# Kernel tuning notes

Measured on AMD Instinct MI355X. Metric: run time of the kernel, lower is better.

Reference implementation:

```python
import jax, jax.numpy as jnp
import numpy as np

B, S, D, H, FF = 4, 1024, 1024, 16, 4096
DH = D // H
EPS = 1e-5


def setup_inputs() -> dict:
    key = jax.random.key(0)
    ks = jax.random.split(key, 24)
    w = lambda i, shp: jax.random.normal(ks[i], shp, jnp.float32) * 0.02
    inp = {
        'tgt': jax.random.normal(ks[0], (B, S, D), jnp.float32),
        'memory': jax.random.normal(ks[1], (B, S, D), jnp.float32),
        'mask': jax.random.randint(ks[2], (B, S, S), 0, 2, jnp.int32),
        # self-attention projections (stored [in,out]; torch Linear weight transposed)
        'sa_wq': w(3, (D, D)), 'sa_bq': jnp.zeros((D,), jnp.float32),
        'sa_wk': w(4, (D, D)), 'sa_bk': jnp.zeros((D,), jnp.float32),
        'sa_wv': w(5, (D, D)), 'sa_bv': jnp.zeros((D,), jnp.float32),
        'sa_wo': w(6, (D, D)), 'sa_bo': jnp.zeros((D,), jnp.float32),
        # cross-attention projections
        'ca_wq': w(7, (D, D)), 'ca_bq': jnp.zeros((D,), jnp.float32),
        'ca_wk': w(8, (D, D)), 'ca_bk': jnp.zeros((D,), jnp.float32),
        'ca_wv': w(9, (D, D)), 'ca_bv': jnp.zeros((D,), jnp.float32),
        'ca_wo': w(10, (D, D)), 'ca_bo': jnp.zeros((D,), jnp.float32),
        # FFN
        'w1': w(11, (D, FF)), 'b1': jnp.zeros((FF,), jnp.float32),
        'w2': w(12, (FF, D)), 'b2': jnp.zeros((D,), jnp.float32),
        # LayerNorms
        'g1': jnp.ones((D,), jnp.float32), 'be1': jnp.zeros((D,), jnp.float32),
        'g2': jnp.ones((D,), jnp.float32), 'be2': jnp.zeros((D,), jnp.float32),
        'g3': jnp.ones((D,), jnp.float32), 'be3': jnp.zeros((D,), jnp.float32),
    }
    return inp


def _layernorm(x, g, b):
    m = jnp.mean(x, axis=-1, keepdims=True)
    v = jnp.mean((x - m) ** 2, axis=-1, keepdims=True)
    return (x - m) * jax.lax.rsqrt(v + EPS) * g + b


def _mha(x, y, mask, wq, bq, wk, bk, wv, bv, wo, bo):
    # chunk(h,-1)+cat(0) head-split == reshape to [B,S,H,DH]
    b_, sq, _ = x.shape
    sk = y.shape[1]
    q = (x @ wq + bq).reshape(b_, sq, H, DH)
    k = (y @ wk + bk).reshape(b_, sk, H, DH)
    v = (y @ wv + bv).reshape(b_, sk, H, DH)
    score = jnp.einsum('bqhd,bkhd->bhqk', q, k) / jnp.float32(np.sqrt(DH))
    score = score + (1.0 - mask[:, None].astype(score.dtype)) * (-1e9)
    attn = jax.nn.softmax(score, axis=-1)
    out = jnp.einsum('bhqk,bkhd->bqhd', attn, v).reshape(b_, sq, D)
    return out @ wo + bo


def reference(tgt, memory, mask,
              sa_wq, sa_bq, sa_wk, sa_bk, sa_wv, sa_bv, sa_wo, sa_bo,
              ca_wq, ca_bq, ca_wk, ca_bk, ca_wv, ca_bv, ca_wo, ca_bo,
              w1, b1, w2, b2, g1, be1, g2, be2, g3, be3):
    t = tgt + _mha(tgt, tgt, mask, sa_wq, sa_bq, sa_wk, sa_bk, sa_wv, sa_bv, sa_wo, sa_bo)
    t = _layernorm(t, g1, be1)
    t = t + _mha(t, memory, mask, ca_wq, ca_bq, ca_wk, ca_bk, ca_wv, ca_bv, ca_wo, ca_bo)
    t = _layernorm(t, g2, be2)
    t = t + (jax.nn.relu(t @ w1 + b1) @ w2 + b2)
    t = _layernorm(t, g3, be3)
    return t
```

## Files before the change

### kernel.cpp

```cpp
#include <hip/hip_runtime.h>
#include <math.h>

typedef float f32x4 __attribute__((ext_vector_type(4)));
typedef unsigned short ushort8 __attribute__((ext_vector_type(8)));
typedef unsigned short ushort4v __attribute__((ext_vector_type(4)));
typedef __bf16 bf16x8 __attribute__((ext_vector_type(8)));
typedef unsigned int u32;

__device__ __forceinline__ unsigned short f2bf(float x) {
  union { float f; unsigned u; } v; v.f = x;
  unsigned r = v.u + 0x7FFFu + ((v.u >> 16) & 1u);
  return (unsigned short)(r >> 16);
}
__device__ __forceinline__ float bf2f(unsigned short u) {
  union { unsigned u; float f; } c; c.u = ((unsigned)u) << 16; return c.f;
}

__device__ __forceinline__ f32x4 mfma16(ushort8 a, ushort8 b, f32x4 c) {
  return __builtin_amdgcn_mfma_f32_16x16x32_bf16(
      __builtin_bit_cast(bf16x8, a), __builtin_bit_cast(bf16x8, b), c, 0, 0, 0);
}

__device__ __forceinline__ void gload16(const void* g, void* l) {
  __builtin_amdgcn_global_load_lds((const __attribute__((address_space(1))) u32*)g,
                                   (__attribute__((address_space(3))) u32*)l, 16, 0, 0);
}

__device__ __forceinline__ int xcd_swz(int orig, int nwg) {
  int q = nwg >> 3, r = nwg & 7;
  int xcd = orig & 7, lid = orig >> 3;
  return (xcd < r ? xcd * (q + 1) : r * (q + 1) + (xcd - r) * q) + lid;
}

__global__ __launch_bounds__(256) void gemm_bf16_kernel(
    const unsigned short* __restrict__ A, const unsigned short* __restrict__ Bt,
    const float* __restrict__ bias, void* __restrict__ C,
    int M, int N, int K, int flags)
{
  __shared__ __align__(16) char As0[128 * 128];
  __shared__ __align__(16) char Bs0[128 * 128];
  __shared__ __align__(16) char As1[128 * 128];
  __shared__ __align__(16) char Bs1[128 * 128];
  const int gx = gridDim.x;
  const int wg = xcd_swz(blockIdx.x + gx * blockIdx.y, gx * gridDim.y);
  const int bn = wg % gx, bm = wg / gx;
  const int z = blockIdx.z;
  const int t = threadIdx.x;
  const int lane = t & 63, w = t >> 6, wm = w >> 1, wn = w & 1;
  const int l4 = lane & 15, lg = lane >> 4;
  const size_t K2 = (size_t)K * 2;

  f32x4 acc[4][4];
#pragma unroll
  for (int i = 0; i < 4; ++i)
#pragma unroll
    for (int j = 0; j < 4; ++j) acc[i][j] = f32x4{0.f, 0.f, 0.f, 0.f};

  const int lr = lane >> 3;
  const int ls = (lane & 7) ^ lr;
  const char* Ag = (const char*)A + (size_t)(bm * 128 + w * 32 + lr) * K2 + ls * 16;
  const char* Bg = (const char*)Bt + (size_t)(bn * 128 + w * 32 + lr) * K2 + ls * 16;
  const int wo = w * 4096;

  auto STAGE = [&](char* Al, char* Bl, int kt) {
    const size_t ko = (size_t)kt * 128;
#pragma unroll
    for (int i = 0; i < 4; ++i) {
      gload16(Ag + i * 8 * K2 + ko, Al + wo + i * 1024);
      gload16(Bg + i * 8 * K2 + ko, Bl + wo + i * 1024);
    }
  };
  auto COMPUTE = [&](const char* As, const char* Bs) {
#pragma unroll
    for (int ks = 0; ks < 2; ++ks) {
      const int kb = ks * 64 + lg * 16;
      ushort8 af[4], bfr[4];
#pragma unroll
      for (int mi = 0; mi < 4; ++mi) {
        int r = wm * 64 + mi * 16 + l4;
        af[mi] = *reinterpret_cast<const ushort8*>(As + r * 128 + (kb ^ ((r & 7) << 4)));
      }
#pragma unroll
      for (int ni = 0; ni < 4; ++ni) {
        int r = wn * 64 + ni * 16 + l4;
        bfr[ni] = *reinterpret_cast<const ushort8*>(Bs + r * 128 + (kb ^ ((r & 7) << 4)));
      }
#pragma unroll
      for (int mi = 0; mi < 4; ++mi)
#pragma unroll
        for (int ni = 0; ni < 4; ++ni)
          acc[mi][ni] = mfma16(af[mi], bfr[ni], acc[mi][ni]);
    }
  };

#define GWAIT(more) do { if (more) asm volatile("s_waitcnt vmcnt(8)" ::: "memory"); \
                         else      asm volatile("s_waitcnt vmcnt(0)" ::: "memory"); } while (0)

  const int nkt2 = (K >> 6) / gridDim.z;
  const int kbeg = z * nkt2, kend = kbeg + nkt2;
  STAGE(As0, Bs0, kbeg);
  STAGE(As1, Bs1, kbeg + 1);
  for (int kt = kbeg; kt < kend; kt += 2) {
    GWAIT(kt + 1 < kend);
    __builtin_amdgcn_s_barrier();
    __builtin_amdgcn_sched_barrier(0);
    COMPUTE(As0, Bs0);
    __builtin_amdgcn_s_barrier();
    __builtin_amdgcn_sched_barrier(0);
    if (kt + 2 < kend) STAGE(As0, Bs0, kt + 2);
    GWAIT(kt + 2 < kend);
    __builtin_amdgcn_s_barrier();
    __builtin_amdgcn_sched_barrier(0);
    COMPUTE(As1, Bs1);
    __builtin_amdgcn_s_barrier();
    __builtin_amdgcn_sched_barrier(0);
    if (kt + 3 < kend) STAGE(As1, Bs1, kt + 3);
  }
#undef GWAIT

  const int relu = flags & 1, obf = flags & 2;
#pragma unroll
  for (int mi = 0; mi < 4; ++mi)
#pragma unroll
    for (int ni = 0; ni < 4; ++ni) {
      int col = bn * 128 + wn * 64 + ni * 16 + l4;
      float bia = (z == 0) ? bias[col] : 0.f;
#pragma unroll
      for (int j = 0; j < 4; ++j) {
        int row = bm * 128 + wm * 64 + mi * 16 + lg * 4 + j;
        float vv = acc[mi][ni][j] + bia;
        if (relu) vv = fmaxf(vv, 0.f);
        size_t idx = (size_t)z * M * N + (size_t)row * N + col;
        if (obf) ((unsigned short*)C)[idx] = f2bf(vv);
        else     ((float*)C)[idx] = vv;
      }
    }
}

constexpr int kS = 1024, kD = 1024, kDH = 64;

__global__ __launch_bounds__(256) void attn_kernel(
    const unsigned short* __restrict__ Qg, const unsigned short* __restrict__ Kg,
    const unsigned short* __restrict__ Vg, int qs, int ks_,
    const unsigned short* __restrict__ mpack, unsigned short* __restrict__ Og)
{
  __shared__ __align__(16) char Ks0[8192];
  __shared__ __align__(16) char Ks1[8192];
  __shared__ __align__(16) char VT0[8192];
  __shared__ __align__(16) char VT1[8192];
  __shared__ __align__(16) char Ps[8192];
  const int wg = xcd_swz(blockIdx.x + 16 * (blockIdx.y + 16 * blockIdx.z), 1024);
  const int qt = wg & 15, h = (wg >> 4) & 15, b = wg >> 8;
  const int t = threadIdx.x, lane = t & 63, w = t >> 6;
  const int l4 = lane & 15, lg = lane >> 4;
  const int lr = lane >> 3, sg = (lane & 7) ^ lr;

  ushort8 q0, q1;
  {
    const unsigned short* src = Qg + (size_t)(b * kS + qt * 64 + w * 16 + l4) * qs + h * kDH;
    q0 = *reinterpret_cast<const ushort8*>(src + lg * 8);
    q1 = *reinterpret_cast<const ushort8*>(src + 32 + lg * 8);
  }
  const unsigned short* mtb = mpack + (size_t)(b * 16 + qt) * 4096 + t;

  auto stageK = [&](char* Kl, int kt) {
    const char* base = (const char*)(Kg + (size_t)(b * kS + kt * 64) * ks_ + h * kDH) + sg * 16;
    gload16(base + (size_t)(w * 16 + lr) * (ks_ * 2), Kl + w * 2048);
    gload16(base + (size_t)(w * 16 + 8 + lr) * (ks_ * 2), Kl + w * 2048 + 1024);
  };

  float m_r[4], l_p[4];
  f32x4 o[4];
#pragma unroll
  for (int j = 0; j < 4; ++j) { m_r[j] = -1e30f; l_p[j] = 0.f; }
#pragma unroll
  for (int di = 0; di < 4; ++di) o[di] = f32x4{0.f, 0.f, 0.f, 0.f};

  ushort8 vA0, vA1, vB0, vB1;
  unsigned short mA, mB;
  stageK(Ks0, 0);
  {
    const unsigned short* vsrc = Vg + (size_t)(b * kS + (t >> 2)) * ks_ + h * kDH + (t & 3) * 16;
    vA0 = *reinterpret_cast<const ushort8*>(vsrc);
    vA1 = *reinterpret_cast<const ushort8*>(vsrc + 8);
    mA = mtb[0];
  }

#define ATTN_TILE(KC, VC, KN, VC0, VC1, VN0, VN1, MCUR, MNXT, KTV)                       \
  {                                                                                      \
    asm volatile("s_waitcnt vmcnt(0)" ::: "memory");                                     \
    {       \
      int key2 = (t >> 2) * 2, c0 = (t & 3) * 16;                                        \
      _Pragma("unroll")                                                                  \
      for (int i = 0; i < 8; ++i) {                                                      \
        int dh = c0 + i;                                                                 \
        *(unsigned short*)(VC + dh * 128 +                                               \
            (key2 ^ ((dh & 7) << 4) ^ ((dh >> 4) << 5))) = VC0[i];                       \
      }                                                                                  \
      _Pragma("unroll")                                                                  \
      for (int i = 0; i < 8; ++i) {                                                      \
        int dh = c0 + 8 + i;                                                             \
        *(unsigned short*)(VC + dh * 128 +                                               \
            (key2 ^ ((dh & 7) << 4) ^ ((dh >> 4) << 5))) = VC1[i];                       \
      }                                                                                  \
    }                                                                                    \
    asm volatile("s_waitcnt lgkmcnt(0)" ::: "memory");                                   \
    __builtin_amdgcn_s_barrier();                                                        \
    __builtin_amdgcn_sched_barrier(0);                                                   \
    if ((KTV) + 1 < 16) {                  \
      stageK(KN, (KTV) + 1);                                                             \
      const unsigned short* vsrc = Vg +                                                  \
          (size_t)(b * kS + ((KTV) + 1) * 64 + (t >> 2)) * ks_ + h * kDH + (t & 3) * 16; \
      VN0 = *reinterpret_cast<const ushort8*>(vsrc);                                     \
      VN1 = *reinterpret_cast<const ushort8*>(vsrc + 8);                                 \
      MNXT = mtb[((KTV) + 1) * 256];                                                     \
    }                                                                                    \
    f32x4 sc[4];                                                                         \
    _Pragma("unroll")                                                                    \
    for (int ni = 0; ni < 4; ++ni) sc[ni] = f32x4{0.f, 0.f, 0.f, 0.f};                   \
    __builtin_amdgcn_s_setprio(1);                                                       \
    _Pragma("unroll")                                                                    \
    for (int ks = 0; ks < 2; ++ks) {                                                     \
      const int kb = ks * 64 + lg * 16;                                                  \
      ushort8 a = ks ? q1 : q0;                                                          \
      _Pragma("unroll")                                                                  \
      for (int ni = 0; ni < 4; ++ni) {                                                   \
        int kr = ni * 16 + l4;                                                           \
        ushort8 bb = *(const ushort8*)(KC + kr * 128 + (kb ^ ((kr & 7) << 4)));          \
        sc[ni] = mfma16(a, bb, sc[ni]);                                                  \
      }                                                                                  \
    }                                                                                    \
    __builtin_amdgcn_s_setprio(0);                                                       \
    const unsigned mbits_ = (unsigned)(MCUR);                                            \
    float tmax[4];                                                                       \
    _Pragma("unroll")                                                                    \
    for (int j = 0; j < 4; ++j) {                                                        \
      _Pragma("unroll")                                                                  \
      for (int ni = 0; ni < 4; ++ni)                                                     \
        if (!((mbits_ >> (ni * 4 + j)) & 1u)) sc[ni][j] = -1e9f;                         \
      tmax[j] = fmaxf(fmaxf(sc[0][j], sc[1][j]), fmaxf(sc[2][j], sc[3][j]));             \
    }                                                                                    \
    bool need = (tmax[0] > m_r[0] + 8.f) || (tmax[1] > m_r[1] + 8.f) ||                  \
                (tmax[2] > m_r[2] + 8.f) || (tmax[3] > m_r[3] + 8.f);                    \
    if (__any(need)) {                 \
      _Pragma("unroll")                                                                  \
      for (int j = 0; j < 4; ++j) {                                                      \
        tmax[j] = fmaxf(tmax[j], __shfl_xor(tmax[j], 1, 64));                            \
        tmax[j] = fmaxf(tmax[j], __shfl_xor(tmax[j], 2, 64));                            \
        tmax[j] = fmaxf(tmax[j], __shfl_xor(tmax[j], 4, 64));                            \
        tmax[j] = fmaxf(tmax[j], __shfl_xor(tmax[j], 8, 64));                            \
        float mn = fmaxf(m_r[j], tmax[j]);                                               \
        float al = exp2f(m_r[j] - mn);                                                   \
        m_r[j] = mn; l_p[j] *= al;                                                       \
        o[0][j] *= al; o[1][j] *= al; o[2][j] *= al; o[3][j] *= al;                      \
      }                                                                                  \
    }                                                                                    \
    _Pragma("unroll")                                                                    \
    for (int ni = 0; ni < 4; ++ni)                                                       \
      _Pragma("unroll")                                                                  \
      for (int j = 0; j < 4; ++j) {                                                      \
        float p = exp2f(sc[ni][j] - m_r[j]);                                             \
        sc[ni][j] = p;                                                                   \
        l_p[j] += p;                                                                     \
      }                                                                                  \
    {                               \
      char* Pw = Ps + w * 2048;                                                          \
      _Pragma("unroll")                                                                  \
      for (int ni = 0; ni < 4; ++ni)                                                     \
        _Pragma("unroll")                                                                \
        for (int j = 0; j < 4; ++j) {                                                    \
          int row = lg * 4 + j, col = ni * 16 + l4;                                      \
          *(unsigned short*)(Pw + row * 128 +                                            \
              ((col * 2) ^ ((row & 7) << 4) ^ ((row & 8) << 2))) =                       \
              __builtin_bit_cast(unsigned short, (__bf16)sc[ni][j]);                     \
        }                                                                                \
    }                                                                                    \
    asm volatile("s_waitcnt lgkmcnt(0)" ::: "memory");                                   \
    __builtin_amdgcn_sched_barrier(0);                                                   \
    __builtin_amdgcn_s_setprio(1);                                                       \
    {                      \
      const char* Pw = Ps + w * 2048;                                                    \
      _Pragma("unroll")                                                                  \
      for (int ks = 0; ks < 2; ++ks) {                                                   \
        const int kb = ks * 64 + lg * 16;                                                \
        ushort8 pa = *(const ushort8*)(Pw + l4 * 128 +                                   \
            (kb ^ ((l4 & 7) << 4) ^ ((l4 & 8) << 2)));                                   \
        _Pragma("unroll")                                                                \
        for (int di = 0; di < 4; ++di) {                                                 \
          int vr2 = di * 16 + l4;                                                        \
          ushort8 vb = *(const ushort8*)(VC + vr2 * 128 +                                \
              (kb ^ ((vr2 & 7) << 4) ^ ((vr2 >> 4) << 5)));                              \
          o[di] = mfma16(pa, vb, o[di]);                                                 \
        }                                                                                \
      }                                                                                  \
    }                                                                                    \
    __builtin_amdgcn_s_setprio(0);                                                       \
  }

  for (int kt = 0; kt < 16; kt += 2) {
    ATTN_TILE(Ks0, VT0, Ks1, vA0, vA1, vB0, vB1, mA, mB, kt);
    ATTN_TILE(Ks1, VT1, Ks0, vB0, vB1, vA0, vA1, mB, mA, kt + 1);
  }
#undef ATTN_TILE

  float rinv[4];
#pragma unroll
  for (int j = 0; j < 4; ++j) {
    float s = l_p[j];
    s += __shfl_xor(s, 1, 64);
    s += __shfl_xor(s, 2, 64);
    s += __shfl_xor(s, 4, 64);
    s += __shfl_xor(s, 8, 64);
    rinv[j] = 1.0f / s;
  }
#pragma unroll
  for (int di = 0; di < 4; ++di) {
    int col = h * kDH + di * 16 + l4;
#pragma unroll
    for (int j = 0; j < 4; ++j) {
      int qrow = qt * 64 + w * 16 + lg * 4 + j;
      Og[(size_t)(b * kS + qrow) * kD + col] =
          __builtin_bit_cast(unsigned short, (__bf16)(o[di][j] * rinv[j]));
    }
  }
}

__global__ __launch_bounds__(256) void addln_kernel(
    const float* __restrict__ x, const unsigned short* __restrict__ y0,
    const unsigned short* __restrict__ y1,
    const float* __restrict__ g, const float* __restrict__ be,
    float* __restrict__ out, unsigned short* __restrict__ ob)
{
  const int row = blockIdx.x, t = threadIdx.x;
  const size_t base = (size_t)row * 1024 + t * 4;
  float4 xv = *reinterpret_cast<const float4*>(x + base);
  ushort4v yv0 = *reinterpret_cast<const ushort4v*>(y0 + base);
  ushort4v yv1 = *reinterpret_cast<const ushort4v*>(y1 + base);
  float v0 = xv.x + bf2f(yv0[0]) + bf2f(yv1[0]);
  float v1 = xv.y + bf2f(yv0[1]) + bf2f(yv1[1]);
  float v2 = xv.z + bf2f(yv0[2]) + bf2f(yv1[2]);
  float v3 = xv.w + bf2f(yv0[3]) + bf2f(yv1[3]);
  float s1 = v0 + v1 + v2 + v3;
  float s2 = v0 * v0 + v1 * v1 + v2 * v2 + v3 * v3;
#pragma unroll
  for (int off = 1; off < 64; off <<= 1) {
    s1 += __shfl_xor(s1, off, 64);
    s2 += __shfl_xor(s2, off, 64);
  }
  __shared__ float r1[4], r2[4];
  const int w = t >> 6, lane = t & 63;
  if (lane == 0) { r1[w] = s1; r2[w] = s2; }
  __syncthreads();
  s1 = r1[0] + r1[1] + r1[2] + r1[3];
  s2 = r2[0] + r2[1] + r2[2] + r2[3];
  const float mean = s1 * (1.0f / 1024.0f);
  const float var = s2 * (1.0f / 1024.0f) - mean * mean;
  const float rs = rsqrtf(var + 1e-5f);
  float4 gv = *reinterpret_cast<const float4*>(g + t * 4);
  float4 bv = *reinterpret_cast<const float4*>(be + t * 4);
  float4 ov;
  ov.x = (v0 - mean) * rs * gv.x + bv.x;
  ov.y = (v1 - mean) * rs * gv.y + bv.y;
  ov.z = (v2 - mean) * rs * gv.z + bv.z;
  ov.w = (v3 - mean) * rs * gv.w + bv.w;
  *reinterpret_cast<float4*>(out + base) = ov;
  if (ob) {
    ushort4v bo;
    bo[0] = f2bf(ov.x); bo[1] = f2bf(ov.y); bo[2] = f2bf(ov.z); bo[3] = f2bf(ov.w);
    *reinterpret_cast<ushort4v*>(ob + base) = bo;
  }
}

__global__ __launch_bounds__(256) void cvt2_bf16_kernel(
    const float* __restrict__ a, const float* __restrict__ b,
    unsigned short* __restrict__ da, unsigned short* __restrict__ db, int n8each)
{
  int i = blockIdx.x * 256 + threadIdx.x;
  const float* s = a; unsigned short* d = da;
  if (i >= n8each) { s = b; d = db; i -= n8each; }
  if (i >= n8each) return;
  float4 f0 = reinterpret_cast<const float4*>(s)[i * 2];
  float4 f1 = reinterpret_cast<const float4*>(s)[i * 2 + 1];
  ushort8 v;
  v[0] = f2bf(f0.x); v[1] = f2bf(f0.y); v[2] = f2bf(f0.z); v[3] = f2bf(f0.w);
  v[4] = f2bf(f1.x); v[5] = f2bf(f1.y); v[6] = f2bf(f1.z); v[7] = f2bf(f1.w);
  reinterpret_cast<ushort8*>(d)[i] = v;
}

__global__ __launch_bounds__(256) void transpose_cvt_kernel(
    const float* __restrict__ src, unsigned short* __restrict__ dst, int K, int N)
{
  __shared__ float tile[32][33];
  const int bx = blockIdx.x, by = blockIdx.y;
  const int tx = threadIdx.x & 31, ty = threadIdx.x >> 5;
#pragma unroll
  for (int i = 0; i < 4; ++i)
    tile[ty + i * 8][tx] = src[(size_t)(by * 32 + ty + i * 8) * N + bx * 32 + tx];
  __syncthreads();
#pragma unroll
  for (int i = 0; i < 4; ++i)
    dst[(size_t)(bx * 32 + ty + i * 8) * K + by * 32 + tx] = f2bf(tile[tx][ty + i * 8]);
}

struct TPtrs { const float* s[8]; unsigned short* d[8]; float scale[8]; };
__global__ __launch_bounds__(256) void tcvt_batch_kernel(TPtrs p)
{
  __shared__ float tile[32][33];
  const float* __restrict__ src = p.s[blockIdx.z];
  unsigned short* __restrict__ dst = p.d[blockIdx.z];
  const float sc = p.scale[blockIdx.z];
  const int bx = blockIdx.x, by = blockIdx.y;
  const int tx = threadIdx.x & 31, ty = threadIdx.x >> 5;
#pragma unroll
  for (int i = 0; i < 4; ++i)
    tile[ty + i * 8][tx] = src[(size_t)(by * 32 + ty + i * 8) * 1024 + bx * 32 + tx];
  __syncthreads();
#pragma unroll
  for (int i = 0; i < 4; ++i)
    dst[(size_t)(bx * 32 + ty + i * 8) * 1024 + by * 32 + tx] = f2bf(tile[tx][ty + i * 8] * sc);
}

__global__ void biasprep_kernel(const float* sq, const float* sk, const float* sv,
                                const float* cq, const float* ck, const float* cv,
                                float* bsa, float* bca, float* bcq, float s)
{
  int i = blockIdx.x * 256 + threadIdx.x;
  if (i < 1024) { bsa[i] = sq[i] * s; bcq[i] = cq[i] * s; bca[i] = ck[i]; bca[i + 1024] = cv[i]; }
  else if (i < 2048) bsa[i] = sk[i - 1024];
  else if (i < 3072) bsa[i] = sv[i - 2048];
}

__global__ __launch_bounds__(256) void maskprep_kernel(
    const int* __restrict__ mask, unsigned short* __restrict__ mpack)
{
  int idx = blockIdx.x * 256 + threadIdx.x;
  int t = idx & 255;
  int kt = (idx >> 8) & 15;
  int qt = (idx >> 12) & 15;
  int b = idx >> 16;
  int qb = qt * 64 + ((t >> 6) & 3) * 16 + ((t >> 4) & 3) * 4;
  int kb = kt * 64 + (t & 15);
  unsigned m = 0;
#pragma unroll
  for (int ni = 0; ni < 4; ++ni)
#pragma unroll
    for (int j = 0; j < 4; ++j)
      if (mask[(size_t)(b * 1024 + qb + j) * 1024 + kb + ni * 16]) m |= 1u << (ni * 4 + j);
  mpack[idx] = (unsigned short)m;
}

__global__ void zfill_kernel(unsigned short* dst, int n8) {
  int i = blockIdx.x * 256 + threadIdx.x;
  if (i < n8) reinterpret_cast<ushort8*>(dst)[i] = ushort8{0,0,0,0,0,0,0,0};
}

extern "C" void kernel_launch(void* const* d_in, const int* in_sizes, int n_in,
                              void* d_out, int out_size, void* d_ws, size_t ws_size,
                              hipStream_t stream)
{
  const float* tgt  = (const float*)d_in[0];
  const float* memi = (const float*)d_in[1];
  const int*   mask = (const int*)d_in[2];
  const float* sa_wq = (const float*)d_in[3];  const float* sa_bq = (const float*)d_in[4];
  const float* sa_wk = (const float*)d_in[5];  const float* sa_bk = (const float*)d_in[6];
  const float* sa_wv = (const float*)d_in[7];  const float* sa_bv = (const float*)d_in[8];
  const float* sa_wo = (const float*)d_in[9];  const float* sa_bo = (const float*)d_in[10];
  const float* ca_wq = (const float*)d_in[11]; const float* ca_bq = (const float*)d_in[12];
  const float* ca_wk = (const float*)d_in[13]; const float* ca_bk = (const float*)d_in[14];
  const float* ca_wv = (const float*)d_in[15]; const float* ca_bv = (const float*)d_in[16];
  const float* ca_wo = (const float*)d_in[17]; const float* ca_bo = (const float*)d_in[18];
  const float* w1 = (const float*)d_in[19]; const float* b1 = (const float*)d_in[20];
  const float* w2 = (const float*)d_in[21]; const float* b2 = (const float*)d_in[22];
  const float* g1 = (const float*)d_in[23]; const float* be1 = (const float*)d_in[24];
  const float* g2 = (const float*)d_in[25]; const float* be2 = (const float*)d_in[26];
  const float* g3 = (const float*)d_in[27]; const float* be3 = (const float*)d_in[28];
  float* out = (float*)d_out;
  char* W = (char*)d_ws;
  const size_t MB = 1 << 20;
  typedef unsigned short us;
  const float QSCALE = 0.18033688011112042f;

  us* Wsaqkv = (us*)(W + 0);
  us* Wsao   = (us*)(W + 6 * MB);
  us* Wcaq   = (us*)(W + 8 * MB);
  us* Wcakv  = (us*)(W + 10 * MB);
  us* Wcao   = (us*)(W + 14 * MB);
  us* W1t    = (us*)(W + 16 * MB);
  us* W2t    = (us*)(W + 24 * MB);
  float* b_saqkv = (float*)(W + 32 * MB);
  float* b_cakv  = (float*)(W + 32 * MB + 16384);
  float* b_caq   = (float*)(W + 32 * MB + 32768);
  us* tgt_bf = (us*)(W + 33 * MB);
  us* T2b    = tgt_bf;
  us* mem_bf = (us*)(W + 41 * MB);
  us* QKV    = (us*)(W + 49 * MB);
  us* Qca    = (us*)(W + 49 * MB);
  us* KVca   = (us*)(W + 57 * MB);
  us* T1b    = (us*)(W + 65 * MB);
  us* AO     = (us*)(W + 73 * MB);
  us* Hb     = (us*)(W + 49 * MB);
  us* Opb    = (us*)(W + 81 * MB);
  us* mpack  = (us*)(W + 97 * MB);
  float* T1f = (float*)(W + 98 * MB);
  float* T2f = T1f;
  us* Opb1   = Opb + 4096 * 1024;

  const int M = 4096;
  dim3 blk(256);
  auto gemm = [&](const us* Aa, const us* Bta, const float* bias, void* Cc,
                  int Nn, int Kk, int flags, int zsplit) {
    gemm_bf16_kernel<<<dim3(Nn / 128, M / 128, zsplit), blk, 0, stream>>>(
        Aa, Bta, bias, Cc, M, Nn, Kk, flags);
  };

  TPtrs tp;
  tp.s[0] = sa_wq; tp.d[0] = Wsaqkv;              tp.scale[0] = QSCALE;
  tp.s[1] = sa_wk; tp.d[1] = Wsaqkv + 1024 * 1024; tp.scale[1] = 1.f;
  tp.s[2] = sa_wv; tp.d[2] = Wsaqkv + 2048 * 1024; tp.scale[2] = 1.f;
  tp.s[3] = sa_wo; tp.d[3] = Wsao;                 tp.scale[3] = 1.f;
  tp.s[4] = ca_wq; tp.d[4] = Wcaq;                 tp.scale[4] = QSCALE;
  tp.s[5] = ca_wk; tp.d[5] = Wcakv;                tp.scale[5] = 1.f;
  tp.s[6] = ca_wv; tp.d[6] = Wcakv + 1024 * 1024;  tp.scale[6] = 1.f;
  tp.s[7] = ca_wo; tp.d[7] = Wcao;                 tp.scale[7] = 1.f;
  tcvt_batch_kernel<<<dim3(32, 32, 8), blk, 0, stream>>>(tp);
  transpose_cvt_kernel<<<dim3(128, 32), blk, 0, stream>>>(w1, W1t, 1024, 4096);
  transpose_cvt_kernel<<<dim3(32, 128), blk, 0, stream>>>(w2, W2t, 4096, 1024);
  cvt2_bf16_kernel<<<dim3(4096), blk, 0, stream>>>(tgt, memi, tgt_bf, mem_bf, M * 1024 / 8);
  biasprep_kernel<<<dim3(12), blk, 0, stream>>>(sa_bq, sa_bk, sa_bv, ca_bq, ca_bk, ca_bv,
                                                b_saqkv, b_cakv, b_caq, QSCALE);
  maskprep_kernel<<<dim3(1024), blk, 0, stream>>>(mask, mpack);

  gemm(tgt_bf, Wsaqkv, b_saqkv, QKV, 3072, 1024, 2, 1);
  attn_kernel<<<dim3(16, 16, 4), blk, 0, stream>>>(QKV, QKV + 1024, QKV + 2048, 3072, 3072, mpack, AO);
  gemm(AO, Wsao, sa_bo, Opb, 1024, 1024, 2, 2);
  addln_kernel<<<dim3(M), blk, 0, stream>>>(tgt, Opb, Opb1, g1, be1, T1f, T1b);

  gemm(T1b, Wcaq, b_caq, Qca, 1024, 1024, 2, 1);
  gemm(mem_bf, Wcakv, b_cakv, KVca, 2048, 1024, 2, 1);
  attn_kernel<<<dim3(16, 16, 4), blk, 0, stream>>>(Qca, KVca, KVca + 1024, 1024, 2048, mpack, AO);
  gemm(AO, Wcao, ca_bo, Opb, 1024, 1024, 2, 2);
  addln_kernel<<<dim3(M), blk, 0, stream>>>(T1f, Opb, Opb1, g2, be2, T2f, T2b);

  gemm(T2b, W1t, b1, Hb, 4096, 1024, 3, 1);
  gemm(Hb, W2t, b2, Opb, 1024, 4096, 2, 2);
  addln_kernel<<<dim3(M), blk, 0, stream>>>(T2f, Opb, Opb1, g3, be3, out, nullptr);

  (void)in_sizes; (void)n_in; (void)out_size; (void)ws_size;
}
```

Baseline: 398.1 us.

## Fuse cross-attn Q/KV GEMMs, use MFMA row sums, keep residuals bf16

```diff
diff --git a/kernel.cpp b/kernel.cpp
--- a/kernel.cpp
+++ b/kernel.cpp
@@ -33,7 +33,8 @@
 }
 
 __global__ __launch_bounds__(256) void gemm_bf16_kernel(
-    const unsigned short* __restrict__ A, const unsigned short* __restrict__ Bt,
+    const unsigned short* __restrict__ A, const unsigned short* __restrict__ A2,
+    int nsplit, const unsigned short* __restrict__ Bt,
     const float* __restrict__ bias, void* __restrict__ C,
     int M, int N, int K, int flags)
 {
@@ -58,7 +59,8 @@
 
   const int lr = lane >> 3;
   const int ls = (lane & 7) ^ lr;
-  const char* Ag = (const char*)A + (size_t)(bm * 128 + w * 32 + lr) * K2 + ls * 16;
+  const unsigned short* Ause = (bn < nsplit) ? A : A2;
+  const char* Ag = (const char*)Ause + (size_t)(bm * 128 + w * 32 + lr) * K2 + ls * 16;
   const char* Bg = (const char*)Bt + (size_t)(bn * 128 + w * 32 + lr) * K2 + ls * 16;
   const int wo = w * 4096;
 
@@ -161,6 +163,10 @@
     q0 = *reinterpret_cast<const ushort8*>(src + lg * 8);
     q1 = *reinterpret_cast<const ushort8*>(src + 32 + lg * 8);
   }
+  ushort8 onesv;
+#pragma unroll
+  for (int i = 0; i < 8; ++i) onesv[i] = 0x3F80;
+
   const unsigned short* mtb = mpack + (size_t)(b * 16 + qt) * 4096 + t;
 
   auto stageK = [&](char* Kl, int kt) {
@@ -169,10 +175,11 @@
     gload16(base + (size_t)(w * 16 + 8 + lr) * (ks_ * 2), Kl + w * 2048 + 1024);
   };
 
-  float m_r[4], l_p[4];
+  float m_r[4];
+  f32x4 l_acc = f32x4{0.f, 0.f, 0.f, 0.f};
   f32x4 o[4];
 #pragma unroll
-  for (int j = 0; j < 4; ++j) { m_r[j] = -1e30f; l_p[j] = 0.f; }
+  for (int j = 0; j < 4; ++j) m_r[j] = -1e30f;
 #pragma unroll
   for (int di = 0; di < 4; ++di) o[di] = f32x4{0.f, 0.f, 0.f, 0.f};
 
@@ -251,18 +258,16 @@
         tmax[j] = fmaxf(tmax[j], __shfl_xor(tmax[j], 8, 64));                            \
         float mn = fmaxf(m_r[j], tmax[j]);                                               \
         float al = exp2f(m_r[j] - mn);                                                   \
-        m_r[j] = mn; l_p[j] *= al;                                                       \
+        m_r[j] = mn;                                                                     \
         o[0][j] *= al; o[1][j] *= al; o[2][j] *= al; o[3][j] *= al;                      \
+        l_acc[j] *= al;                                                                  \
       }                                                                                  \
     }                                                                                    \
     _Pragma("unroll")                                                                    \
     for (int ni = 0; ni < 4; ++ni)                                                       \
       _Pragma("unroll")                                                                  \
-      for (int j = 0; j < 4; ++j) {                                                      \
-        float p = exp2f(sc[ni][j] - m_r[j]);                                             \
-        sc[ni][j] = p;                                                                   \
-        l_p[j] += p;                                                                     \
-      }                                                                                  \
+      for (int j = 0; j < 4; ++j)                                                        \
+        sc[ni][j] = exp2f(sc[ni][j] - m_r[j]);                                           \
     {                               \
       char* Pw = Ps + w * 2048;                                                          \
       _Pragma("unroll")                                                                  \
@@ -278,13 +283,14 @@
     asm volatile("s_waitcnt lgkmcnt(0)" ::: "memory");                                   \
     __builtin_amdgcn_sched_barrier(0);                                                   \
     __builtin_amdgcn_s_setprio(1);                                                       \
-    {                      \
+    {                                             \
       const char* Pw = Ps + w * 2048;                                                    \
       _Pragma("unroll")                                                                  \
       for (int ks = 0; ks < 2; ++ks) {                                                   \
         const int kb = ks * 64 + lg * 16;                                                \
         ushort8 pa = *(const ushort8*)(Pw + l4 * 128 +                                   \
             (kb ^ ((l4 & 7) << 4) ^ ((l4 & 8) << 2)));                                   \
+        l_acc = mfma16(pa, onesv, l_acc);                                                \
         _Pragma("unroll")                                                                \
         for (int di = 0; di < 4; ++di) {                                                 \
           int vr2 = di * 16 + l4;                                                        \
@@ -305,14 +311,7 @@
 
   float rinv[4];
 #pragma unroll
-  for (int j = 0; j < 4; ++j) {
-    float s = l_p[j];
-    s += __shfl_xor(s, 1, 64);
-    s += __shfl_xor(s, 2, 64);
-    s += __shfl_xor(s, 4, 64);
-    s += __shfl_xor(s, 8, 64);
-    rinv[j] = 1.0f / s;
-  }
+  for (int j = 0; j < 4; ++j) rinv[j] = 1.0f / l_acc[j];
 #pragma unroll
   for (int di = 0; di < 4; ++di) {
     int col = h * kDH + di * 16 + l4;
@@ -326,20 +325,20 @@
 }
 
 __global__ __launch_bounds__(256) void addln_kernel(
-    const float* __restrict__ x, const unsigned short* __restrict__ y0,
+    const unsigned short* __restrict__ x, const unsigned short* __restrict__ y0,
     const unsigned short* __restrict__ y1,
     const float* __restrict__ g, const float* __restrict__ be,
-    float* __restrict__ out, unsigned short* __restrict__ ob)
+    unsigned short* __restrict__ outb, float* __restrict__ outf)
 {
   const int row = blockIdx.x, t = threadIdx.x;
   const size_t base = (size_t)row * 1024 + t * 4;
-  float4 xv = *reinterpret_cast<const float4*>(x + base);
+  ushort4v xv = *reinterpret_cast<const ushort4v*>(x + base);
   ushort4v yv0 = *reinterpret_cast<const ushort4v*>(y0 + base);
   ushort4v yv1 = *reinterpret_cast<const ushort4v*>(y1 + base);
-  float v0 = xv.x + bf2f(yv0[0]) + bf2f(yv1[0]);
-  float v1 = xv.y + bf2f(yv0[1]) + bf2f(yv1[1]);
-  float v2 = xv.z + bf2f(yv0[2]) + bf2f(yv1[2]);
-  float v3 = xv.w + bf2f(yv0[3]) + bf2f(yv1[3]);
+  float v0 = bf2f(xv[0]) + bf2f(yv0[0]) + bf2f(yv1[0]);
+  float v1 = bf2f(xv[1]) + bf2f(yv0[1]) + bf2f(yv1[1]);
+  float v2 = bf2f(xv[2]) + bf2f(yv0[2]) + bf2f(yv1[2]);
+  float v3 = bf2f(xv[3]) + bf2f(yv0[3]) + bf2f(yv1[3]);
   float s1 = v0 + v1 + v2 + v3;
   float s2 = v0 * v0 + v1 * v1 + v2 * v2 + v3 * v3;
 #pragma unroll
@@ -363,12 +362,12 @@
   ov.y = (v1 - mean) * rs * gv.y + bv.y;
   ov.z = (v2 - mean) * rs * gv.z + bv.z;
   ov.w = (v3 - mean) * rs * gv.w + bv.w;
-  *reinterpret_cast<float4*>(out + base) = ov;
-  if (ob) {
+  if (outb) {
     ushort4v bo;
     bo[0] = f2bf(ov.x); bo[1] = f2bf(ov.y); bo[2] = f2bf(ov.z); bo[3] = f2bf(ov.w);
-    *reinterpret_cast<ushort4v*>(ob + base) = bo;
-  }
+    *reinterpret_cast<ushort4v*>(outb + base) = bo;
+  }
+  if (outf) *reinterpret_cast<float4*>(outf + base) = ov;
 }
 
 __global__ __launch_bounds__(256) void cvt2_bf16_kernel(
@@ -422,12 +421,12 @@
 
 __global__ void biasprep_kernel(const float* sq, const float* sk, const float* sv,
                                 const float* cq, const float* ck, const float* cv,
-                                float* bsa, float* bca, float* bcq, float s)
+                                float* bsa, float* bca, float s)
 {
   int i = blockIdx.x * 256 + threadIdx.x;
-  if (i < 1024) { bsa[i] = sq[i] * s; bcq[i] = cq[i] * s; bca[i] = ck[i]; bca[i + 1024] = cv[i]; }
-  else if (i < 2048) bsa[i] = sk[i - 1024];
-  else if (i < 3072) bsa[i] = sv[i - 2048];
+  if (i < 1024)      { bsa[i] = sq[i] * s;        bca[i] = cq[i] * s; }
+  else if (i < 2048) { bsa[i] = sk[i - 1024];     bca[i] = ck[i - 1024]; }
+  else if (i < 3072) { bsa[i] = sv[i - 2048];     bca[i] = cv[i - 2048]; }
 }
 
 __global__ __launch_bounds__(256) void maskprep_kernel(
@@ -447,11 +446,6 @@
     for (int j = 0; j < 4; ++j)
       if (mask[(size_t)(b * 1024 + qb + j) * 1024 + kb + ni * 16]) m |= 1u << (ni * 4 + j);
   mpack[idx] = (unsigned short)m;
-}
-
-__global__ void zfill_kernel(unsigned short* dst, int n8) {
-  int i = blockIdx.x * 256 + threadIdx.x;
-  if (i < n8) reinterpret_cast<ushort8*>(dst)[i] = ushort8{0,0,0,0,0,0,0,0};
 }
 
 extern "C" void kernel_launch(void* const* d_in, const int* in_sizes, int n_in,
@@ -482,68 +476,61 @@
 
   us* Wsaqkv = (us*)(W + 0);
   us* Wsao   = (us*)(W + 6 * MB);
-  us* Wcaq   = (us*)(W + 8 * MB);
-  us* Wcakv  = (us*)(W + 10 * MB);
+  us* Wcaqkv = (us*)(W + 8 * MB);
   us* Wcao   = (us*)(W + 14 * MB);
   us* W1t    = (us*)(W + 16 * MB);
   us* W2t    = (us*)(W + 24 * MB);
   float* b_saqkv = (float*)(W + 32 * MB);
-  float* b_cakv  = (float*)(W + 32 * MB + 16384);
-  float* b_caq   = (float*)(W + 32 * MB + 32768);
+  float* b_caqkv = (float*)(W + 32 * MB + 16384);
   us* tgt_bf = (us*)(W + 33 * MB);
   us* T2b    = tgt_bf;
   us* mem_bf = (us*)(W + 41 * MB);
   us* QKV    = (us*)(W + 49 * MB);
-  us* Qca    = (us*)(W + 49 * MB);
-  us* KVca   = (us*)(W + 57 * MB);
-  us* T1b    = (us*)(W + 65 * MB);
   us* AO     = (us*)(W + 73 * MB);
   us* Hb     = (us*)(W + 49 * MB);
   us* Opb    = (us*)(W + 81 * MB);
   us* mpack  = (us*)(W + 97 * MB);
-  float* T1f = (float*)(W + 98 * MB);
-  float* T2f = T1f;
+  us* T1b    = (us*)(W + 98 * MB);
   us* Opb1   = Opb + 4096 * 1024;
 
   const int M = 4096;
   dim3 blk(256);
-  auto gemm = [&](const us* Aa, const us* Bta, const float* bias, void* Cc,
-                  int Nn, int Kk, int flags, int zsplit) {
+  auto gemm = [&](const us* Aa, const us* Aa2, int nsplit, const us* Bta,
+                  const float* bias, void* Cc, int Nn, int Kk, int flags, int zsplit) {
     gemm_bf16_kernel<<<dim3(Nn / 128, M / 128, zsplit), blk, 0, stream>>>(
-        Aa, Bta, bias, Cc, M, Nn, Kk, flags);
+        Aa, Aa2, nsplit, Bta, bias, Cc, M, Nn, Kk, flags);
   };
 
   TPtrs tp;
-  tp.s[0] = sa_wq; tp.d[0] = Wsaqkv;              tp.scale[0] = QSCALE;
+  tp.s[0] = sa_wq; tp.d[0] = Wsaqkv;               tp.scale[0] = QSCALE;
   tp.s[1] = sa_wk; tp.d[1] = Wsaqkv + 1024 * 1024; tp.scale[1] = 1.f;
   tp.s[2] = sa_wv; tp.d[2] = Wsaqkv + 2048 * 1024; tp.scale[2] = 1.f;
   tp.s[3] = sa_wo; tp.d[3] = Wsao;                 tp.scale[3] = 1.f;
-  tp.s[4] = ca_wq; tp.d[4] = Wcaq;                 tp.scale[4] = QSCALE;
-  tp.s[5] = ca_wk; tp.d[5] = Wcakv;                tp.scale[5] = 1.f;
-  tp.s[6] = ca_wv; tp.d[6] = Wcakv + 1024 * 1024;  tp.scale[6] = 1.f;
+  tp.s[4] = ca_wq; tp.d[4] = Wcaqkv;               tp.scale[4] = QSCALE;
+  tp.s[5] = ca_wk; tp.d[5] = Wcaqkv + 1024 * 1024; tp.scale[5] = 1.f;
+  tp.s[6] = ca_wv; tp.d[6] = Wcaqkv + 2048 * 1024; tp.scale[6] = 1.f;
   tp.s[7] = ca_wo; tp.d[7] = Wcao;                 tp.scale[7] = 1.f;
   tcvt_batch_kernel<<<dim3(32, 32, 8), blk, 0, stream>>>(tp);
   transpose_cvt_kernel<<<dim3(128, 32), blk, 0, stream>>>(w1, W1t, 1024, 4096);
   transpose_cvt_kernel<<<dim3(32, 128), blk, 0, stream>>>(w2, W2t, 4096, 1024);
   cvt2_bf16_kernel<<<dim3(4096), blk, 0, stream>>>(tgt, memi, tgt_bf, mem_bf, M * 1024 / 8);
   biasprep_kernel<<<dim3(12), blk, 0, stream>>>(sa_bq, sa_bk, sa_bv, ca_bq, ca_bk, ca_bv,
-                                                b_saqkv, b_cakv, b_caq, QSCALE);
+                                                b_saqkv, b_caqkv, QSCALE);
   maskprep_kernel<<<dim3(1024), blk, 0, stream>>>(mask, mpack);
 
-  gemm(tgt_bf, Wsaqkv, b_saqkv, QKV, 3072, 1024, 2, 1);
+  gemm(tgt_bf, tgt_bf, 1 << 30, Wsaqkv, b_saqkv, QKV, 3072, 1024, 2, 1);
   attn_kernel<<<dim3(16, 16, 4), blk, 0, stream>>>(QKV, QKV + 1024, QKV + 2048, 3072, 3072, mpack, AO);
-  gemm(AO, Wsao, sa_bo, Opb, 1024, 1024, 2, 2);
-  addln_kernel<<<dim3(M), blk, 0, stream>>>(tgt, Opb, Opb1, g1, be1, T1f, T1b);
-
-  gemm(T1b, Wcaq, b_caq, Qca, 1024, 1024, 2, 1);
-  gemm(mem_bf, Wcakv, b_cakv, KVca, 2048, 1024, 2, 1);
-  attn_kernel<<<dim3(16, 16, 4), blk, 0, stream>>>(Qca, KVca, KVca + 1024, 1024, 2048, mpack, AO);
-  gemm(AO, Wcao, ca_bo, Opb, 1024, 1024, 2, 2);
-  addln_kernel<<<dim3(M), blk, 0, stream>>>(T1f, Opb, Opb1, g2, be2, T2f, T2b);
-
-  gemm(T2b, W1t, b1, Hb, 4096, 1024, 3, 1);
-  gemm(Hb, W2t, b2, Opb, 1024, 4096, 2, 2);
-  addln_kernel<<<dim3(M), blk, 0, stream>>>(T2f, Opb, Opb1, g3, be3, out, nullptr);
+  gemm(AO, AO, 1 << 30, Wsao, sa_bo, Opb, 1024, 1024, 2, 2);
+  addln_kernel<<<dim3(M), blk, 0, stream>>>(tgt_bf, Opb, Opb1, g1, be1, T1b, nullptr);
+
+  gemm(T1b, mem_bf, 8, Wcaqkv, b_caqkv, QKV, 3072, 1024, 2, 1);
+  attn_kernel<<<dim3(16, 16, 4), blk, 0, stream>>>(QKV, QKV + 1024, QKV + 2048, 3072, 3072, mpack, AO);
+  gemm(AO, AO, 1 << 30, Wcao, ca_bo, Opb, 1024, 1024, 2, 2);
+  addln_kernel<<<dim3(M), blk, 0, stream>>>(T1b, Opb, Opb1, g2, be2, T2b, nullptr);
+
+  gemm(T2b, T2b, 1 << 30, W1t, b1, Hb, 4096, 1024, 3, 1);
+  gemm(Hb, Hb, 1 << 30, W2t, b2, Opb, 1024, 4096, 2, 2);
+  addln_kernel<<<dim3(M), blk, 0, stream>>>(T2b, Opb, Opb1, g3, be3, nullptr, out);
 
   (void)in_sizes; (void)n_in; (void)out_size; (void)ws_size;
 }
```

Measured after the change: 383.1 us. 1.04x faster.
